# Kernel tuning notes

Measured on AMD Instinct MI355X. Metric: run time of the kernel, lower is better.

Reference implementation:

```python
import jax, jax.numpy as jnp
import numpy as np

B, S, D, DH = 4, 2048, 1024, 64


def setup_inputs() -> dict:
    key = jax.random.key(0)
    ks = jax.random.split(key, 7)
    x = jax.random.normal(ks[0], (B, S, D), dtype=jnp.float32)
    def w(k):
        return jax.random.normal(k, (D, DH), dtype=jnp.float32) / np.sqrt(D).astype(np.float32)
    return {
        'x': x,
        'w_q_u': w(ks[1]), 'w_k_u': w(ks[2]), 'w_v_u': w(ks[3]),
        'w_q_c': w(ks[4]), 'w_k_c': w(ks[5]), 'w_v_c': w(ks[6]),
    }


def reference(x, w_q_u, w_k_u, w_v_u, w_q_c, w_k_c, w_v_c):
    b, n, _ = x.shape
    scale = w_q_u.shape[-1] ** -0.5
    # projections (LinearNoBias -> plain matmul)
    Q_u = x @ w_q_u
    K_u = x @ w_k_u
    V_u = x @ w_v_u
    Q_c = x @ w_q_c
    K_c = x @ w_k_c
    V_c = x @ w_v_c

    i = jnp.arange(n)
    causal = i[:, None] >= i[None, :]        # True where j <= i (binary causal / keep for S_c)
    lookahead = i[:, None] < i[None, :]      # True where j > i (allowed in sigmoid term)

    # term1: [b, n, n], zeroed above the diagonal via binary causal mask
    term1 = jnp.einsum('bid,bjd->bij', Q_c, V_u) * scale * causal.astype(x.dtype)

    # sigmoid gate: lookahead mask adds -inf on/below the diagonal -> sigmoid = 0 there
    logits_u = jnp.einsum('bid,bjd->bij', Q_u, K_u) * scale
    sigmoid_term = jax.nn.sigmoid(jnp.where(lookahead, logits_u, -jnp.inf))

    # nested n^3 matmul: S_u[b,i,k] = sum_j term1[b,i,j] * sigmoid_term[b,k,j]
    S_u = jnp.einsum('bij,bkj->bik', term1, sigmoid_term)

    S_c = jnp.where(causal, jnp.einsum('bid,bjd->bij', Q_c, K_c) * scale, -jnp.inf)

    attn = jax.nn.softmax(S_c - jax.nn.silu(S_u), axis=-1)
    return jnp.einsum('bij,bjd->bid', attn, V_c)
```

## Files before the change

kernel.cpp:

```cpp
#include <hip/hip_runtime.h>
#include <hip/hip_bf16.h>

typedef short bf16x8 __attribute__((ext_vector_type(8)));
typedef float f32x4  __attribute__((ext_vector_type(4)));
typedef _Float16 f16x8 __attribute__((ext_vector_type(8)));

#define MFMA16(a,b,c)  __builtin_amdgcn_mfma_f32_16x16x32_bf16((a),(b),(c),0,0,0)
#define MFMAF16(a,b,c) __builtin_amdgcn_mfma_f32_16x16x32_f16((a),(b),(c),0,0,0)

#define GLDS16(g,l) __builtin_amdgcn_global_load_lds( \
    (const __attribute__((address_space(1))) void*)(g), \
    (__attribute__((address_space(3))) void*)(l), 16, 0, 0)

__device__ __forceinline__ short f2bf(float f){
  union { float f; unsigned u; } v; v.f = f;
  unsigned r = v.u + 0x7fffu + ((v.u >> 16) & 1u);
  return (short)(r >> 16);
}
__device__ __forceinline__ float bf2f(short h){
  union { unsigned u; float f; } v; v.u = ((unsigned)(unsigned short)h) << 16;
  return v.f;
}
__device__ __forceinline__ void split8v(f32x4 a, f32x4 b, bf16x8& h, bf16x8& l){
  float t[8] = {a[0],a[1],a[2],a[3],b[0],b[1],b[2],b[3]};
  #pragma unroll
  for (int e = 0; e < 8; ++e){
    short hs = f2bf(t[e]);
    h[e] = hs;
    l[e] = f2bf(t[e] - bf2f(hs));
  }
}

__global__ void k_wt(const float* w0, const float* w1, const float* w2,
                     const float* w3, const float* w4, const float* w5,
                     unsigned short* __restrict__ wth, unsigned short* __restrict__ wtl){
  int p = blockIdx.y;
  const float* wp = p==0?w0:p==1?w1:p==2?w2:p==3?w3:p==4?w4:w5;
  int idx = blockIdx.x*256 + threadIdx.x;
  int n = idx >> 10, k = idx & 1023;
  float v = wp[k*64 + n];
  short hs = f2bf(v);
  wth[(size_t)p*65536 + n*1024 + k] = (unsigned short)hs;
  wtl[(size_t)p*65536 + n*1024 + k] = (unsigned short)f2bf(v - bf2f(hs));
}

__global__ void k_xsplit(const float* __restrict__ x,
                         unsigned short* __restrict__ xh, unsigned short* __restrict__ xl){
  size_t i = ((size_t)blockIdx.x*256 + threadIdx.x)*8;
  f32x4 a = *(const f32x4*)(x + i);
  f32x4 b = *(const f32x4*)(x + i + 4);
  bf16x8 h, l;
  split8v(a, b, h, l);
  *(bf16x8*)(xh + i) = h;
  *(bf16x8*)(xl + i) = l;
}

__global__ __launch_bounds__(256) void k_proj(
    const unsigned short* __restrict__ xh, const unsigned short* __restrict__ xl,
    const unsigned short* __restrict__ wth, const unsigned short* __restrict__ wtl,
    float* __restrict__ proj,
    unsigned short* __restrict__ projh, unsigned short* __restrict__ projl){
  __shared__ __align__(16) char sm[49152];
  int blk = blockIdx.x;
  int rb = blk/3, pg = blk - rb*3;
  int tid = threadIdx.x, w = tid >> 6, lane = tid & 63;
  int lm = lane & 15, quad = lane >> 4;
  int srow = lane >> 3, scg = (lane & 7) ^ srow;
  const char* xhg = (const char*)xh;
  const char* xlg = (const char*)xl;
  const char* w0h = (const char*)wth + (size_t)(pg*2  )*131072;
  const char* w0l = (const char*)wtl + (size_t)(pg*2  )*131072;
  const char* w1h = (const char*)wth + (size_t)(pg*2+1)*131072;
  const char* w1l = (const char*)wtl + (size_t)(pg*2+1)*131072;
  f32x4 acc[2][4] = {};
  for (int k0 = 0; k0 < 1024; k0 += 64){
    __syncthreads();
    size_t cb = (size_t)k0*2 + scg*16;
    #pragma unroll
    for (int i2 = 0; i2 < 2; ++i2){
      int i = w*2 + i2;
      size_t gx = (size_t)(rb*64 + i*8 + srow)*2048 + cb;
      size_t gw = (size_t)(i*8 + srow)*2048 + cb;
      GLDS16(xhg + gx, sm +         i*1024);
      GLDS16(xlg + gx, sm +  8192 + i*1024);
      GLDS16(w0h + gw, sm + 16384 + i*1024);
      GLDS16(w0l + gw, sm + 24576 + i*1024);
      GLDS16(w1h + gw, sm + 32768 + i*1024);
      GLDS16(w1l + gw, sm + 40960 + i*1024);
    }
    __syncthreads();
    #pragma unroll
    for (int ks = 0; ks < 2; ++ks){
      int ra = w*16 + lm;
      int offa = ra*128 + (((ks*4+quad) ^ (ra&7))*16);
      bf16x8 ah = *(const bf16x8*)(sm + offa);
      bf16x8 al = *(const bf16x8*)(sm + 8192 + offa);
      #pragma unroll
      for (int sub = 0; sub < 2; ++sub){
        #pragma unroll
        for (int n = 0; n < 4; ++n){
          int r = n*16 + lm;
          int off = r*128 + (((ks*4+quad) ^ (r&7))*16);
          bf16x8 bh = *(const bf16x8*)(sm + 16384 + sub*16384 + off);
          bf16x8 bl = *(const bf16x8*)(sm + 24576 + sub*16384 + off);
          acc[sub][n] = MFMA16(ah, bh, acc[sub][n]);
          acc[sub][n] = MFMA16(ah, bl, acc[sub][n]);
          acc[sub][n] = MFMA16(al, bh, acc[sub][n]);
        }
      }
    }
  }
  #pragma unroll
  for (int sub = 0; sub < 2; ++sub){
    int p = pg*2 + sub;
    if (p == 5){
      float* op = proj + (size_t)5*524288;
      #pragma unroll
      for (int n = 0; n < 4; ++n)
        #pragma unroll
        for (int e = 0; e < 4; ++e){
          int r = rb*64 + w*16 + quad*4 + e;
          op[(size_t)r*64 + n*16 + lm] = acc[sub][n][e];
        }
    } else {
      unsigned short* oph = projh + (size_t)p*524288;
      unsigned short* opl = projl + (size_t)p*524288;
      #pragma unroll
      for (int n = 0; n < 4; ++n)
        #pragma unroll
        for (int e = 0; e < 4; ++e){
          int r = rb*64 + w*16 + quad*4 + e;
          float f = acc[sub][n][e];
          short hs = f2bf(f);
          oph[(size_t)r*64 + n*16 + lm] = (unsigned short)hs;
          opl[(size_t)r*64 + n*16 + lm] = (unsigned short)f2bf(f - bf2f(hs));
        }
    }
  }
}

__global__ void k_vct(const float* __restrict__ proj, _Float16* __restrict__ vct){
  __shared__ float T[64][65];
  int b = blockIdx.y, st = blockIdx.x;
  int tid = threadIdx.x;
  const float* vc = proj + 5*524288 + (size_t)b*131072;
  int sloc = tid >> 2, cp = (tid & 3)*16;
  #pragma unroll
  for (int j = 0; j < 4; ++j){
    f32x4 v = *(const f32x4*)(vc + (size_t)(st*64 + sloc)*64 + cp + j*4);
    #pragma unroll
    for (int e = 0; e < 4; ++e) T[sloc][cp + j*4 + e] = v[e];
  }
  __syncthreads();
  int d = tid >> 2, sp = (tid & 3)*16;
  f16x8 h0, h1;
  #pragma unroll
  for (int j = 0; j < 8; ++j) h0[j] = (_Float16)T[sp + j][d];
  #pragma unroll
  for (int j = 0; j < 8; ++j) h1[j] = (_Float16)T[sp + 8 + j][d];
  size_t o = (size_t)b*131072 + (size_t)d*2048 + st*64 + sp;
  *(f16x8*)(vct + o) = h0; *(f16x8*)(vct + o + 8) = h1;
}

__global__ __launch_bounds__(256,2) void k_p2(
    const unsigned short* __restrict__ ph, const unsigned short* __restrict__ pl,
    _Float16* __restrict__ t1, _Float16* __restrict__ sg){
  __shared__ __align__(16) char sm[65536];
  int b = blockIdx.y;
  int t = blockIdx.x;
  bool isSig = t >= 136;
  if (isSig) t -= 136;
  int a = 0, bb = 0;
  #pragma unroll 1
  for (int aa = 0; aa < 16; ++aa){
    int c = isSig ? (16 - aa) : (aa + 1);
    if (t < c){ a = aa; bb = isSig ? (aa + t) : t; break; }
    t -= c;
  }
  int pa = isSig ? 0 : 3;
  int pb = isSig ? 1 : 2;
  const char* Ahg = (const char*)ph + (size_t)pa*1048576;
  const char* Alg = (const char*)pl + (size_t)pa*1048576;
  const char* Bhg = (const char*)ph + (size_t)pb*1048576;
  const char* Blg = (const char*)pl + (size_t)pb*1048576;
  int tid = threadIdx.x, w = tid >> 6, lane = tid & 63;
  int lm = lane & 15, quad = lane >> 4;
  int srow = lane >> 3, scg = (lane & 7) ^ srow;
  int wm = (w & 1)*64, wn = (w >> 1)*64;
  #pragma unroll
  for (int i2 = 0; i2 < 4; ++i2){
    int i = w*4 + i2;
    int rl = i*8 + srow;
    size_t ga = (size_t)(b*2048 + a*128  + rl)*128 + scg*16;
    size_t gb = (size_t)(b*2048 + bb*128 + rl)*128 + scg*16;
    GLDS16(Ahg + ga, sm +         i*1024);
    GLDS16(Alg + ga, sm + 16384 + i*1024);
    GLDS16(Bhg + gb, sm + 32768 + i*1024);
    GLDS16(Blg + gb, sm + 49152 + i*1024);
  }
  __syncthreads();
  f32x4 acc[4][4] = {};
  #pragma unroll
  for (int ks = 0; ks < 2; ++ks){
    bf16x8 bh[4], bl[4];
    #pragma unroll
    for (int n = 0; n < 4; ++n){
      int r = wn + n*16 + lm;
      int off = r*128 + (((ks*4+quad) ^ (r&7))*16);
      bh[n] = *(const bf16x8*)(sm + 32768 + off);
      bl[n] = *(const bf16x8*)(sm + 49152 + off);
    }
    #pragma unroll
    for (int m = 0; m < 4; ++m){
      int r = wm + m*16 + lm;
      int off = r*128 + (((ks*4+quad) ^ (r&7))*16);
      bf16x8 ah = *(const bf16x8*)(sm + off);
      bf16x8 al = *(const bf16x8*)(sm + 16384 + off);
      #pragma unroll
      for (int n = 0; n < 4; ++n){
        acc[m][n] = MFMA16(ah, bh[n], acc[m][n]);
        acc[m][n] = MFMA16(ah, bl[n], acc[m][n]);
        acc[m][n] = MFMA16(al, bh[n], acc[m][n]);
      }
    }
  }
  __syncthreads();
  _Float16* Tt = (_Float16*)sm;
  #pragma unroll
  for (int m = 0; m < 4; ++m){
    #pragma unroll
    for (int n = 0; n < 4; ++n){
      #pragma unroll
      for (int e = 0; e < 4; ++e){
        int il = wm + m*16 + quad*4 + e;
        int jl = wn + n*16 + lm;
        int gi = a*128 + il, gj = bb*128 + jl;
        float v = acc[m][n][e] * 0.125f;
        float outv;
        if (!isSig) outv = (gj <= gi) ? v : 0.0f;
        else        outv = (gj >  gi) ? (1.0f/(1.0f + __expf(-v))) : 0.0f;
        Tt[il*128 + jl] = (_Float16)outv;
      }
    }
  }
  __syncthreads();
  _Float16* outp = (isSig ? sg : t1) + (size_t)b*4194304;
  #pragma unroll
  for (int r = 0; r < 8; ++r){
    int lrow = w*32 + r*4 + (lane >> 4);
    int c16 = lane & 15;
    f32x4 vv = *(const f32x4*)(sm + lrow*256 + c16*16);
    *(f32x4*)((char*)(outp + (size_t)(a*128 + lrow)*2048 + bb*128) + c16*16) = vv;
  }
}

__global__ __launch_bounds__(256,2) void k_p3(
    const unsigned short* __restrict__ ph, const unsigned short* __restrict__ pl,
    const _Float16* __restrict__ t1, const _Float16* __restrict__ sg,
    _Float16* __restrict__ lg){
  __shared__ __align__(16) char sm[65536];
  int b = blockIdx.y;
  int v = blockIdx.x, I = 0, K = 0;
  #pragma unroll 1
  for (int d = 15; d >= 0; --d){
    int nd = 16 - d;
    if (v < nd){ I = d + v; K = v; break; }
    v -= nd;
  }
  int tid = threadIdx.x, w = tid >> 6, lane = tid & 63;
  int lm = lane & 15, quad = lane >> 4;
  size_t mat = (size_t)b * 4194304;
  const char* Ag = (const char*)(t1 + mat);
  const char* Bg = (const char*)(sg + mat);
  int srow = lane >> 3, scg = (lane & 7) ^ srow;
  int wm = (w & 1)*64, wn = (w >> 1)*64;
  int nsteps = 2*(I - K) + 2;
  int j0 = 2*K;

  auto stage = [&](int j64, int base){
    size_t colb = (size_t)j64*128 + scg*16;
    #pragma unroll
    for (int i2 = 0; i2 < 4; ++i2){
      int i = w*4 + i2;
      int rl = i*8 + srow;
      GLDS16(Ag + (size_t)(I*128 + rl)*4096 + colb, sm + base +         i*1024);
      GLDS16(Bg + (size_t)(K*128 + rl)*4096 + colb, sm + base + 16384 + i*1024);
    }
  };

  f32x4 su[4][4] = {};
  stage(j0, 0);
  for (int step = 0; step < nsteps; ++step){
    int cur = (step & 1) << 15;
    __syncthreads();
    if (step + 1 < nsteps) stage(j0 + step + 1, (~step & 1) << 15);
    #pragma unroll
    for (int ks = 0; ks < 2; ++ks){
      f16x8 bf[4];
      #pragma unroll
      for (int n = 0; n < 4; ++n){
        int r = wn + n*16 + lm;
        bf[n] = *(const f16x8*)(sm + cur + 16384 + r*128 + (((ks*4+quad) ^ (r&7))*16));
      }
      #pragma unroll
      for (int m = 0; m < 4; ++m){
        int r = wm + m*16 + lm;
        f16x8 af = *(const f16x8*)(sm + cur + r*128 + (((ks*4+quad) ^ (r&7))*16));
        #pragma unroll
        for (int n = 0; n < 4; ++n)
          su[m][n] = MFMAF16(af, bf[n], su[m][n]);
      }
    }
  }
  const char* Qh = (const char*)ph + (size_t)3*1048576;
  const char* Ql = (const char*)pl + (size_t)3*1048576;
  const char* Kh = (const char*)ph + (size_t)4*1048576;
  const char* Kl = (const char*)pl + (size_t)4*1048576;
  f32x4 sc[4][4] = {};
  #pragma unroll
  for (int ks = 0; ks < 2; ++ks){
    bf16x8 kh[4], kl[4];
    #pragma unroll
    for (int n = 0; n < 4; ++n){
      size_t off = (size_t)(b*2048 + K*128 + wn + n*16 + lm)*128 + (ks*32 + quad*8)*2;
      kh[n] = *(const bf16x8*)(Kh + off);
      kl[n] = *(const bf16x8*)(Kl + off);
    }
    #pragma unroll
    for (int m = 0; m < 4; ++m){
      size_t off = (size_t)(b*2048 + I*128 + wm + m*16 + lm)*128 + (ks*32 + quad*8)*2;
      bf16x8 ah = *(const bf16x8*)(Qh + off);
      bf16x8 al = *(const bf16x8*)(Ql + off);
      #pragma unroll
      for (int n = 0; n < 4; ++n){
        sc[m][n] = MFMA16(ah, kh[n], sc[m][n]);
        sc[m][n] = MFMA16(ah, kl[n], sc[m][n]);
        sc[m][n] = MFMA16(al, kh[n], sc[m][n]);
      }
    }
  }
  __syncthreads();
  _Float16* Tt = (_Float16*)sm;
  #pragma unroll
  for (int m = 0; m < 4; ++m){
    #pragma unroll
    for (int n = 0; n < 4; ++n){
      #pragma unroll
      for (int e = 0; e < 4; ++e){
        int il = wm + m*16 + quad*4 + e;
        int jl = wn + n*16 + lm;
        float xv = su[m][n][e];
        float sgm = 1.0f/(1.0f + __expf(-xv));
        Tt[il*128 + jl] = (_Float16)(sc[m][n][e]*0.125f - xv*sgm);
      }
    }
  }
  __syncthreads();
  _Float16* lgb = lg + mat;
  #pragma unroll
  for (int r = 0; r < 8; ++r){
    int lrow = w*32 + r*4 + (lane >> 4);
    int c16 = lane & 15;
    f32x4 vv = *(const f32x4*)(sm + lrow*256 + c16*16);
    *(f32x4*)((char*)(lgb + (size_t)(I*128 + lrow)*2048 + K*128) + c16*16) = vv;
  }
}

__global__ __launch_bounds__(256,2) void k_p4(const _Float16* __restrict__ lg,
    const _Float16* __restrict__ vct, float* __restrict__ out){
  __shared__ __align__(16) char sm[66048];
  float* Mz = (float*)(sm + 65536);
  float* Sz = (float*)(sm + 65792);
  int b = blockIdx.y;
  int band = 127 - blockIdx.x;
  int r0 = band*16;
  int tid = threadIdx.x, w = tid >> 6, lane = tid & 63;
  int lm = lane & 15, quad = lane >> 4;
  const char* lgb = (const char*)lg + ((size_t)b*4194304 + (size_t)r0*2048)*2;
  const _Float16* vb = vct + (size_t)b*131072;
  int nkt = ((r0 + 15) >> 6) + 1;
  int fc = (r0 + 1) >> 6;
  int srl = lane >> 3, ssl = lane & 7;
  for (int kt = w; kt < nkt; kt += 4){
    #pragma unroll
    for (int i2 = 0; i2 < 2; ++i2){
      int rl = i2*8 + srl;
      GLDS16(lgb + (size_t)rl*4096 + kt*128 + ((ssl ^ (rl & 7))*16),
             sm + kt*2048 + i2*1024);
    }
  }
  __syncthreads();
  float m_r = -3.0e38f;
  for (int kt = w; kt < nkt; kt += 4){
    #pragma unroll
    for (int half = 0; half < 2; ++half){
      int sl = quad*2 + half;
      f16x8 v = *(const f16x8*)(sm + kt*2048 + lm*128 + ((sl ^ (lm & 7))*16));
      int cb = kt*64 + sl*8;
      #pragma unroll
      for (int e = 0; e < 8; ++e)
        m_r = (cb + e <= r0 + lm) ? fmaxf(m_r, (float)v[e]) : m_r;
    }
  }
  m_r = fmaxf(m_r, __shfl_xor(m_r, 16));
  m_r = fmaxf(m_r, __shfl_xor(m_r, 32));
  Mz[w*16 + lm] = m_r;
  __syncthreads();
  float mfin = fmaxf(fmaxf(Mz[lm], Mz[16 + lm]), fmaxf(Mz[32 + lm], Mz[48 + lm]));
  float s_r = 0.0f;
  for (int kt = w; kt < nkt; kt += 4){
    #pragma unroll
    for (int half = 0; half < 2; ++half){
      int sl = quad*2 + half;
      f16x8 v = *(const f16x8*)(sm + kt*2048 + lm*128 + ((sl ^ (lm & 7))*16));
      int cb = kt*64 + sl*8;
      #pragma unroll
      for (int e = 0; e < 8; ++e)
        if (cb + e <= r0 + lm) s_r += __expf((float)v[e] - mfin);
    }
  }
  s_r += __shfl_xor(s_r, 16);
  s_r += __shfl_xor(s_r, 32);
  Sz[w*16 + lm] = s_r;
  f32x4 acc[4] = {};
  for (int kt = w; kt < nkt; kt += 4){
    bool full = kt < fc;
    #pragma unroll
    for (int ks = 0; ks < 2; ++ks){
      f16x8 Lv = *(const f16x8*)(sm + kt*2048 + lm*128 + (((ks*4+quad) ^ (lm & 7))*16));
      int jbase = kt*64 + ks*32 + quad*8;
      f16x8 af;
      #pragma unroll
      for (int e = 0; e < 8; ++e){
        float p = __expf((float)Lv[e] - mfin);
        if (!full && (jbase + e > r0 + lm)) p = 0.0f;
        af[e] = (_Float16)p;
      }
      #pragma unroll
      for (int n = 0; n < 4; ++n){
        f16x8 bv = *(const f16x8*)(vb + (size_t)(n*16 + lm)*2048 + jbase);
        acc[n] = MFMAF16(af, bv, acc[n]);
      }
    }
  }
  __syncthreads();
  float* Ot = (float*)sm;
  #pragma unroll
  for (int n = 0; n < 4; ++n)
    #pragma unroll
    for (int e = 0; e < 4; ++e)
      Ot[(w*16 + quad*4 + e)*64 + n*16 + lm] = acc[n][e];
  __syncthreads();
  int row = tid >> 4, c4 = (tid & 15)*4;
  f32x4 s = *(const f32x4*)&Ot[row*64 + c4];
  #pragma unroll
  for (int ww = 1; ww < 4; ++ww){
    f32x4 t2 = *(const f32x4*)&Ot[(ww*16 + row)*64 + c4];
    s[0]+=t2[0]; s[1]+=t2[1]; s[2]+=t2[2]; s[3]+=t2[3];
  }
  float z = Sz[row] + Sz[16 + row] + Sz[32 + row] + Sz[48 + row];
  f32x4 o = { s[0]/z, s[1]/z, s[2]/z, s[3]/z };
  *(f32x4*)(out + ((size_t)b*2048 + r0 + row)*64 + c4) = o;
}

static const size_t OFF_PROJ  = 0;
static const size_t OFF_WTH   = 12582912;
static const size_t OFF_WTL   = 13369344;
static const size_t OFF_PROJH = 14155776;
static const size_t OFF_PROJL = 20447232;
static const size_t OFF_VCT   = 26738688;
static const size_t OFF_T1    = 27787264;
static const size_t OFF_SG    = 61341696;
static const size_t OFF_LG    = 94896128;
static const size_t OFF_XH    = 128450560;
static const size_t OFF_XL    = 145227776;

extern "C" void kernel_launch(void* const* d_in, const int* in_sizes, int n_in,
                              void* d_out, int out_size, void* d_ws, size_t ws_size,
                              hipStream_t stream){
  (void)in_sizes; (void)n_in; (void)out_size; (void)ws_size;
  const float* x = (const float*)d_in[0];
  char* ws = (char*)d_ws;
  float*          proj  = (float*)(ws + OFF_PROJ);
  unsigned short* wth   = (unsigned short*)(ws + OFF_WTH);
  unsigned short* wtl   = (unsigned short*)(ws + OFF_WTL);
  unsigned short* projh = (unsigned short*)(ws + OFF_PROJH);
  unsigned short* projl = (unsigned short*)(ws + OFF_PROJL);
  _Float16*       vct   = (_Float16*)(ws + OFF_VCT);
  _Float16*       t1    = (_Float16*)(ws + OFF_T1);
  _Float16*       sg    = (_Float16*)(ws + OFF_SG);
  _Float16*       lg    = (_Float16*)(ws + OFF_LG);
  unsigned short* xh    = (unsigned short*)(ws + OFF_XH);
  unsigned short* xl    = (unsigned short*)(ws + OFF_XL);

  k_wt    <<<dim3(256,6),  256, 0, stream>>>((const float*)d_in[1], (const float*)d_in[2],
                                             (const float*)d_in[3], (const float*)d_in[4],
                                             (const float*)d_in[5], (const float*)d_in[6], wth, wtl);
  k_xsplit<<<dim3(4096),   256, 0, stream>>>(x, xh, xl);
  k_proj  <<<dim3(384),    256, 0, stream>>>(xh, xl, wth, wtl, proj, projh, projl);
  k_vct   <<<dim3(32,4),   256, 0, stream>>>(proj, vct);
  k_p2    <<<dim3(272,4),  256, 0, stream>>>(projh, projl, t1, sg);
  k_p3    <<<dim3(136,4),  256, 0, stream>>>(projh, projl, t1, sg, lg);
  k_p4    <<<dim3(128,4),  256, 0, stream>>>(lg, vct, (float*)d_out);
}
```

Before: 218.6 us.

## Load-balance causal tile work via host-built bins and paired row bands

k_p3 now launches 64 blocks per batch, and each block loops over a list of (I,K) tiles. The lists are assigned on the host by a greedy scheme that balances the causal triangular K-loop lengths across blocks. k_p4 is also halved to 64 blocks, each processing two complementary row bands (short plus long) so per-block work is even. This aims to remove tail imbalance from the triangular work, at the cost of fewer blocks (256 per kernel), so machine occupancy may be lower and parallelism across CUs reduced.

```diff
diff --git a/kernel.cpp b/kernel.cpp
--- a/kernel.cpp
+++ b/kernel.cpp
@@ -11,6 +11,8 @@
 #define GLDS16(g,l) __builtin_amdgcn_global_load_lds( \
     (const __attribute__((address_space(1))) void*)(g), \
     (__attribute__((address_space(3))) void*)(l), 16, 0, 0)
+
+struct P3Bins { unsigned char cnt[64]; unsigned char tiles[64][14]; };
 
 __device__ __forceinline__ short f2bf(float f){
   union { float f; unsigned u; } v; v.f = f;
@@ -257,16 +259,10 @@
 __global__ __launch_bounds__(256,2) void k_p3(
     const unsigned short* __restrict__ ph, const unsigned short* __restrict__ pl,
     const _Float16* __restrict__ t1, const _Float16* __restrict__ sg,
-    _Float16* __restrict__ lg){
+    _Float16* __restrict__ lg, P3Bins bz){
   __shared__ __align__(16) char sm[65536];
+  int bin = blockIdx.x;
   int b = blockIdx.y;
-  int v = blockIdx.x, I = 0, K = 0;
-  #pragma unroll 1
-  for (int d = 15; d >= 0; --d){
-    int nd = 16 - d;
-    if (v < nd){ I = d + v; K = v; break; }
-    v -= nd;
-  }
   int tid = threadIdx.x, w = tid >> 6, lane = tid & 63;
   int lm = lane & 15, quad = lane >> 4;
   size_t mat = (size_t)b * 4194304;
@@ -274,95 +270,102 @@
   const char* Bg = (const char*)(sg + mat);
   int srow = lane >> 3, scg = (lane & 7) ^ srow;
   int wm = (w & 1)*64, wn = (w >> 1)*64;
-  int nsteps = 2*(I - K) + 2;
-  int j0 = 2*K;
-
-  auto stage = [&](int j64, int base){
-    size_t colb = (size_t)j64*128 + scg*16;
-    #pragma unroll
-    for (int i2 = 0; i2 < 4; ++i2){
-      int i = w*4 + i2;
-      int rl = i*8 + srow;
-      GLDS16(Ag + (size_t)(I*128 + rl)*4096 + colb, sm + base +         i*1024);
-      GLDS16(Bg + (size_t)(K*128 + rl)*4096 + colb, sm + base + 16384 + i*1024);
-    }
-  };
-
-  f32x4 su[4][4] = {};
-  stage(j0, 0);
-  for (int step = 0; step < nsteps; ++step){
-    int cur = (step & 1) << 15;
-    __syncthreads();
-    if (step + 1 < nsteps) stage(j0 + step + 1, (~step & 1) << 15);
+  int ntiles = bz.cnt[bin];
+
+  for (int tix = 0; tix < ntiles; ++tix){
+    int tv = bz.tiles[bin][tix];
+    int I = tv >> 4, K = tv & 15;
+    int nsteps = 2*(I - K) + 2;
+    int j0 = 2*K;
+    __syncthreads();
+
+    auto stage = [&](int j64, int base){
+      size_t colb = (size_t)j64*128 + scg*16;
+      #pragma unroll
+      for (int i2 = 0; i2 < 4; ++i2){
+        int i = w*4 + i2;
+        int rl = i*8 + srow;
+        GLDS16(Ag + (size_t)(I*128 + rl)*4096 + colb, sm + base +         i*1024);
+        GLDS16(Bg + (size_t)(K*128 + rl)*4096 + colb, sm + base + 16384 + i*1024);
+      }
+    };
+
+    f32x4 su[4][4] = {};
+    stage(j0, 0);
+    for (int step = 0; step < nsteps; ++step){
+      int cur = (step & 1) << 15;
+      __syncthreads();
+      if (step + 1 < nsteps) stage(j0 + step + 1, (~step & 1) << 15);
+      #pragma unroll
+      for (int ks = 0; ks < 2; ++ks){
+        f16x8 bf[4];
+        #pragma unroll
+        for (int n = 0; n < 4; ++n){
+          int r = wn + n*16 + lm;
+          bf[n] = *(const f16x8*)(sm + cur + 16384 + r*128 + (((ks*4+quad) ^ (r&7))*16));
+        }
+        #pragma unroll
+        for (int m = 0; m < 4; ++m){
+          int r = wm + m*16 + lm;
+          f16x8 af = *(const f16x8*)(sm + cur + r*128 + (((ks*4+quad) ^ (r&7))*16));
+          #pragma unroll
+          for (int n = 0; n < 4; ++n)
+            su[m][n] = MFMAF16(af, bf[n], su[m][n]);
+        }
+      }
+    }
+    const char* Qh = (const char*)ph + (size_t)3*1048576;
+    const char* Ql = (const char*)pl + (size_t)3*1048576;
+    const char* Kh = (const char*)ph + (size_t)4*1048576;
+    const char* Kl = (const char*)pl + (size_t)4*1048576;
+    f32x4 sc[4][4] = {};
     #pragma unroll
     for (int ks = 0; ks < 2; ++ks){
-      f16x8 bf[4];
+      bf16x8 kh[4], kl[4];
       #pragma unroll
       for (int n = 0; n < 4; ++n){
-        int r = wn + n*16 + lm;
-        bf[n] = *(const f16x8*)(sm + cur + 16384 + r*128 + (((ks*4+quad) ^ (r&7))*16));
+        size_t off = (size_t)(b*2048 + K*128 + wn + n*16 + lm)*128 + (ks*32 + quad*8)*2;
+        kh[n] = *(const bf16x8*)(Kh + off);
+        kl[n] = *(const bf16x8*)(Kl + off);
       }
       #pragma unroll
       for (int m = 0; m < 4; ++m){
-        int r = wm + m*16 + lm;
-        f16x8 af = *(const f16x8*)(sm + cur + r*128 + (((ks*4+quad) ^ (r&7))*16));
-        #pragma unroll
-        for (int n = 0; n < 4; ++n)
-          su[m][n] = MFMAF16(af, bf[n], su[m][n]);
-      }
-    }
-  }
-  const char* Qh = (const char*)ph + (size_t)3*1048576;
-  const char* Ql = (const char*)pl + (size_t)3*1048576;
-  const char* Kh = (const char*)ph + (size_t)4*1048576;
-  const char* Kl = (const char*)pl + (size_t)4*1048576;
-  f32x4 sc[4][4] = {};
-  #pragma unroll
-  for (int ks = 0; ks < 2; ++ks){
-    bf16x8 kh[4], kl[4];
-    #pragma unroll
-    for (int n = 0; n < 4; ++n){
-      size_t off = (size_t)(b*2048 + K*128 + wn + n*16 + lm)*128 + (ks*32 + quad*8)*2;
-      kh[n] = *(const bf16x8*)(Kh + off);
-      kl[n] = *(const bf16x8*)(Kl + off);
-    }
+        size_t off = (size_t)(b*2048 + I*128 + wm + m*16 + lm)*128 + (ks*32 + quad*8)*2;
+        bf16x8 ah = *(const bf16x8*)(Qh + off);
+        bf16x8 al = *(const bf16x8*)(Ql + off);
+        #pragma unroll
+        for (int n = 0; n < 4; ++n){
+          sc[m][n] = MFMA16(ah, kh[n], sc[m][n]);
+          sc[m][n] = MFMA16(ah, kl[n], sc[m][n]);
+          sc[m][n] = MFMA16(al, kh[n], sc[m][n]);
+        }
+      }
+    }
+    __syncthreads();
+    _Float16* Tt = (_Float16*)sm;
     #pragma unroll
     for (int m = 0; m < 4; ++m){
-      size_t off = (size_t)(b*2048 + I*128 + wm + m*16 + lm)*128 + (ks*32 + quad*8)*2;
-      bf16x8 ah = *(const bf16x8*)(Qh + off);
-      bf16x8 al = *(const bf16x8*)(Ql + off);
       #pragma unroll
       for (int n = 0; n < 4; ++n){
-        sc[m][n] = MFMA16(ah, kh[n], sc[m][n]);
-        sc[m][n] = MFMA16(ah, kl[n], sc[m][n]);
-        sc[m][n] = MFMA16(al, kh[n], sc[m][n]);
-      }
-    }
-  }
-  __syncthreads();
-  _Float16* Tt = (_Float16*)sm;
-  #pragma unroll
-  for (int m = 0; m < 4; ++m){
-    #pragma unroll
-    for (int n = 0; n < 4; ++n){
-      #pragma unroll
-      for (int e = 0; e < 4; ++e){
-        int il = wm + m*16 + quad*4 + e;
-        int jl = wn + n*16 + lm;
-        float xv = su[m][n][e];
-        float sgm = 1.0f/(1.0f + __expf(-xv));
-        Tt[il*128 + jl] = (_Float16)(sc[m][n][e]*0.125f - xv*sgm);
-      }
-    }
-  }
-  __syncthreads();
-  _Float16* lgb = lg + mat;
-  #pragma unroll
-  for (int r = 0; r < 8; ++r){
-    int lrow = w*32 + r*4 + (lane >> 4);
-    int c16 = lane & 15;
-    f32x4 vv = *(const f32x4*)(sm + lrow*256 + c16*16);
-    *(f32x4*)((char*)(lgb + (size_t)(I*128 + lrow)*2048 + K*128) + c16*16) = vv;
+        #pragma unroll
+        for (int e = 0; e < 4; ++e){
+          int il = wm + m*16 + quad*4 + e;
+          int jl = wn + n*16 + lm;
+          float xv = su[m][n][e];
+          float sgm = 1.0f/(1.0f + __expf(-xv));
+          Tt[il*128 + jl] = (_Float16)(sc[m][n][e]*0.125f - xv*sgm);
+        }
+      }
+    }
+    __syncthreads();
+    _Float16* lgb = lg + mat;
+    #pragma unroll
+    for (int r = 0; r < 8; ++r){
+      int lrow = w*32 + r*4 + (lane >> 4);
+      int c16 = lane & 15;
+      f32x4 vv = *(const f32x4*)(sm + lrow*256 + c16*16);
+      *(f32x4*)((char*)(lgb + (size_t)(I*128 + lrow)*2048 + K*128) + c16*16) = vv;
+    }
   }
 }
 
@@ -372,95 +375,99 @@
   float* Mz = (float*)(sm + 65536);
   float* Sz = (float*)(sm + 65792);
   int b = blockIdx.y;
-  int band = 127 - blockIdx.x;
-  int r0 = band*16;
+  int b1 = blockIdx.x;
   int tid = threadIdx.x, w = tid >> 6, lane = tid & 63;
   int lm = lane & 15, quad = lane >> 4;
-  const char* lgb = (const char*)lg + ((size_t)b*4194304 + (size_t)r0*2048)*2;
   const _Float16* vb = vct + (size_t)b*131072;
-  int nkt = ((r0 + 15) >> 6) + 1;
-  int fc = (r0 + 1) >> 6;
-  int srl = lane >> 3, ssl = lane & 7;
-  for (int kt = w; kt < nkt; kt += 4){
-    #pragma unroll
-    for (int i2 = 0; i2 < 2; ++i2){
-      int rl = i2*8 + srl;
-      GLDS16(lgb + (size_t)rl*4096 + kt*128 + ((ssl ^ (rl & 7))*16),
-             sm + kt*2048 + i2*1024);
-    }
-  }
-  __syncthreads();
-  float m_r = -3.0e38f;
-  for (int kt = w; kt < nkt; kt += 4){
-    #pragma unroll
-    for (int half = 0; half < 2; ++half){
-      int sl = quad*2 + half;
-      f16x8 v = *(const f16x8*)(sm + kt*2048 + lm*128 + ((sl ^ (lm & 7))*16));
-      int cb = kt*64 + sl*8;
-      #pragma unroll
-      for (int e = 0; e < 8; ++e)
-        m_r = (cb + e <= r0 + lm) ? fmaxf(m_r, (float)v[e]) : m_r;
-    }
-  }
-  m_r = fmaxf(m_r, __shfl_xor(m_r, 16));
-  m_r = fmaxf(m_r, __shfl_xor(m_r, 32));
-  Mz[w*16 + lm] = m_r;
-  __syncthreads();
-  float mfin = fmaxf(fmaxf(Mz[lm], Mz[16 + lm]), fmaxf(Mz[32 + lm], Mz[48 + lm]));
-  float s_r = 0.0f;
-  for (int kt = w; kt < nkt; kt += 4){
-    #pragma unroll
-    for (int half = 0; half < 2; ++half){
-      int sl = quad*2 + half;
-      f16x8 v = *(const f16x8*)(sm + kt*2048 + lm*128 + ((sl ^ (lm & 7))*16));
-      int cb = kt*64 + sl*8;
-      #pragma unroll
-      for (int e = 0; e < 8; ++e)
-        if (cb + e <= r0 + lm) s_r += __expf((float)v[e] - mfin);
-    }
-  }
-  s_r += __shfl_xor(s_r, 16);
-  s_r += __shfl_xor(s_r, 32);
-  Sz[w*16 + lm] = s_r;
-  f32x4 acc[4] = {};
-  for (int kt = w; kt < nkt; kt += 4){
-    bool full = kt < fc;
-    #pragma unroll
-    for (int ks = 0; ks < 2; ++ks){
-      f16x8 Lv = *(const f16x8*)(sm + kt*2048 + lm*128 + (((ks*4+quad) ^ (lm & 7))*16));
-      int jbase = kt*64 + ks*32 + quad*8;
-      f16x8 af;
-      #pragma unroll
-      for (int e = 0; e < 8; ++e){
-        float p = __expf((float)Lv[e] - mfin);
-        if (!full && (jbase + e > r0 + lm)) p = 0.0f;
-        af[e] = (_Float16)p;
-      }
-      #pragma unroll
-      for (int n = 0; n < 4; ++n){
-        f16x8 bv = *(const f16x8*)(vb + (size_t)(n*16 + lm)*2048 + jbase);
-        acc[n] = MFMAF16(af, bv, acc[n]);
-      }
-    }
-  }
-  __syncthreads();
-  float* Ot = (float*)sm;
-  #pragma unroll
-  for (int n = 0; n < 4; ++n)
-    #pragma unroll
-    for (int e = 0; e < 4; ++e)
-      Ot[(w*16 + quad*4 + e)*64 + n*16 + lm] = acc[n][e];
-  __syncthreads();
-  int row = tid >> 4, c4 = (tid & 15)*4;
-  f32x4 s = *(const f32x4*)&Ot[row*64 + c4];
-  #pragma unroll
-  for (int ww = 1; ww < 4; ++ww){
-    f32x4 t2 = *(const f32x4*)&Ot[(ww*16 + row)*64 + c4];
-    s[0]+=t2[0]; s[1]+=t2[1]; s[2]+=t2[2]; s[3]+=t2[3];
-  }
-  float z = Sz[row] + Sz[16 + row] + Sz[32 + row] + Sz[48 + row];
-  f32x4 o = { s[0]/z, s[1]/z, s[2]/z, s[3]/z };
-  *(f32x4*)(out + ((size_t)b*2048 + r0 + row)*64 + c4) = o;
+  for (int pass = 0; pass < 2; ++pass){
+    int band = pass ? (127 - b1) : b1;
+    int r0 = band*16;
+    const char* lgb = (const char*)lg + ((size_t)b*4194304 + (size_t)r0*2048)*2;
+    int nkt = ((r0 + 15) >> 6) + 1;
+    int fc = (r0 + 1) >> 6;
+    int srl = lane >> 3, ssl = lane & 7;
+    __syncthreads();
+    for (int kt = w; kt < nkt; kt += 4){
+      #pragma unroll
+      for (int i2 = 0; i2 < 2; ++i2){
+        int rl = i2*8 + srl;
+        GLDS16(lgb + (size_t)rl*4096 + kt*128 + ((ssl ^ (rl & 7))*16),
+               sm + kt*2048 + i2*1024);
+      }
+    }
+    __syncthreads();
+    float m_r = -3.0e38f;
+    for (int kt = w; kt < nkt; kt += 4){
+      #pragma unroll
+      for (int half = 0; half < 2; ++half){
+        int sl = quad*2 + half;
+        f16x8 v = *(const f16x8*)(sm + kt*2048 + lm*128 + ((sl ^ (lm & 7))*16));
+        int cb = kt*64 + sl*8;
+        #pragma unroll
+        for (int e = 0; e < 8; ++e)
+          m_r = (cb + e <= r0 + lm) ? fmaxf(m_r, (float)v[e]) : m_r;
+      }
+    }
+    m_r = fmaxf(m_r, __shfl_xor(m_r, 16));
+    m_r = fmaxf(m_r, __shfl_xor(m_r, 32));
+    Mz[w*16 + lm] = m_r;
+    __syncthreads();
+    float mfin = fmaxf(fmaxf(Mz[lm], Mz[16 + lm]), fmaxf(Mz[32 + lm], Mz[48 + lm]));
+    float s_r = 0.0f;
+    for (int kt = w; kt < nkt; kt += 4){
+      #pragma unroll
+      for (int half = 0; half < 2; ++half){
+        int sl = quad*2 + half;
+        f16x8 v = *(const f16x8*)(sm + kt*2048 + lm*128 + ((sl ^ (lm & 7))*16));
+        int cb = kt*64 + sl*8;
+        #pragma unroll
+        for (int e = 0; e < 8; ++e)
+          if (cb + e <= r0 + lm) s_r += __expf((float)v[e] - mfin);
+      }
+    }
+    s_r += __shfl_xor(s_r, 16);
+    s_r += __shfl_xor(s_r, 32);
+    Sz[w*16 + lm] = s_r;
+    f32x4 acc[4] = {};
+    for (int kt = w; kt < nkt; kt += 4){
+      bool full = kt < fc;
+      #pragma unroll
+      for (int ks = 0; ks < 2; ++ks){
+        f16x8 Lv = *(const f16x8*)(sm + kt*2048 + lm*128 + (((ks*4+quad) ^ (lm & 7))*16));
+        int jbase = kt*64 + ks*32 + quad*8;
+        f16x8 af;
+        #pragma unroll
+        for (int e = 0; e < 8; ++e){
+          float p = __expf((float)Lv[e] - mfin);
+          if (!full && (jbase + e > r0 + lm)) p = 0.0f;
+          af[e] = (_Float16)p;
+        }
+        #pragma unroll
+        for (int n = 0; n < 4; ++n){
+          f16x8 bv = *(const f16x8*)(vb + (size_t)(n*16 + lm)*2048 + jbase);
+          acc[n] = MFMAF16(af, bv, acc[n]);
+        }
+      }
+    }
+    __syncthreads();
+    float* Ot = (float*)sm;
+    #pragma unroll
+    for (int n = 0; n < 4; ++n)
+      #pragma unroll
+      for (int e = 0; e < 4; ++e)
+        Ot[(w*16 + quad*4 + e)*64 + n*16 + lm] = acc[n][e];
+    __syncthreads();
+    int row = tid >> 4, c4 = (tid & 15)*4;
+    f32x4 s = *(const f32x4*)&Ot[row*64 + c4];
+    #pragma unroll
+    for (int ww = 1; ww < 4; ++ww){
+      f32x4 t2 = *(const f32x4*)&Ot[(ww*16 + row)*64 + c4];
+      s[0]+=t2[0]; s[1]+=t2[1]; s[2]+=t2[2]; s[3]+=t2[3];
+    }
+    float z = Sz[row] + Sz[16 + row] + Sz[32 + row] + Sz[48 + row];
+    f32x4 o = { s[0]/z, s[1]/z, s[2]/z, s[3]/z };
+    *(f32x4*)(out + ((size_t)b*2048 + r0 + row)*64 + c4) = o;
+  }
 }
 
 static const size_t OFF_PROJ  = 0;
@@ -474,6 +481,23 @@
 static const size_t OFF_LG    = 94896128;
 static const size_t OFF_XH    = 128450560;
 static const size_t OFF_XL    = 145227776;
+
+static P3Bins build_bins(){
+  P3Bins bz;
+  int load[64];
+  for (int i = 0; i < 64; ++i){ bz.cnt[i] = 0; load[i] = 0; }
+  for (int d = 15; d >= 0; --d){
+    for (int K = 0; K + d < 16; ++K){
+      int I = K + d;
+      int len = 2*d + 2;
+      int best = 0;
+      for (int bin = 1; bin < 64; ++bin) if (load[bin] < load[best]) best = bin;
+      load[best] += len;
+      bz.tiles[best][bz.cnt[best]++] = (unsigned char)(I*16 + K);
+    }
+  }
+  return bz;
+}
 
 extern "C" void kernel_launch(void* const* d_in, const int* in_sizes, int n_in,
                               void* d_out, int out_size, void* d_ws, size_t ws_size,
@@ -493,6 +517,8 @@
   unsigned short* xh    = (unsigned short*)(ws + OFF_XH);
   unsigned short* xl    = (unsigned short*)(ws + OFF_XL);
 
+  P3Bins bz = build_bins();
+
   k_wt    <<<dim3(256,6),  256, 0, stream>>>((const float*)d_in[1], (const float*)d_in[2],
                                              (const float*)d_in[3], (const float*)d_in[4],
                                              (const float*)d_in[5], (const float*)d_in[6], wth, wtl);
@@ -500,6 +526,6 @@
   k_proj  <<<dim3(384),    256, 0, stream>>>(xh, xl, wth, wtl, proj, projh, projl);
   k_vct   <<<dim3(32,4),   256, 0, stream>>>(proj, vct);
   k_p2    <<<dim3(272,4),  256, 0, stream>>>(projh, projl, t1, sg);
-  k_p3    <<<dim3(136,4),  256, 0, stream>>>(projh, projl, t1, sg, lg);
-  k_p4    <<<dim3(128,4),  256, 0, stream>>>(lg, vct, (float*)d_out);
-}
+  k_p3    <<<dim3(64,4),   256, 0, stream>>>(projh, projl, t1, sg, lg, bz);
+  k_p4    <<<dim3(64,4),   256, 0, stream>>>(lg, vct, (float*)d_out);
+}
```

New measurement: 213.3 us. -2.4%, faster.
